# Kernel optimization log

Hardware: AMD Instinct MI355X
Metric: run time of the kernel (lower is better)

The kernel has to match this reference:

```python
import jax, jax.numpy as jnp
import numpy as np

_EPS = 1e-12  # torch F.normalize eps


def _normalize(x):
    # x: [B, N, 3]; matches torch.nn.functional.normalize(x, dim=2)
    norm = jnp.linalg.norm(x, axis=2, keepdims=True)
    return x / jnp.maximum(norm, _EPS)


def setup_inputs() -> dict:
    key = jax.random.key(0)
    k1, k2 = jax.random.split(key)
    xyz1 = jax.random.normal(k1, (8, 4096, 6), dtype=jnp.float32)
    xyz2 = jax.random.normal(k2, (8, 4096, 6), dtype=jnp.float32)
    return {"xyz1": xyz1, "xyz2": xyz2}


def reference(xyz1, xyz2):
    p1 = xyz1[:, :, :3]  # [B, N, 3]
    p2 = xyz2[:, :, :3]  # [B, M, 3]
    n1 = xyz1[:, :, 3:]  # [B, N, 3]
    n2 = xyz2[:, :, 3:]  # [B, M, 3]

    # Pairwise squared L2: |a|^2 + |b|^2 - 2 a.b  -> [B, N, M]
    sq1 = jnp.sum(p1 * p1, axis=2)  # [B, N]
    sq2 = jnp.sum(p2 * p2, axis=2)  # [B, M]
    cross = jnp.einsum('bnd,bmd->bnm', p1, p2)
    d = sq1[:, :, None] + sq2[:, None, :] - 2.0 * cross  # [B, N, M]

    dist1 = jnp.min(d, axis=2)      # [B, N] NN of each p1 in p2
    idx1 = jnp.argmin(d, axis=2)    # [B, N]
    dist2 = jnp.min(d, axis=1)      # [B, M] NN of each p2 in p1
    idx2 = jnp.argmin(d, axis=1)    # [B, M]

    # Gather matched normals
    t1 = jnp.take_along_axis(n2, idx1[:, :, None], axis=1)  # [B, N, 3]
    t2 = jnp.take_along_axis(n1, idx2[:, :, None], axis=1)  # [B, M, 3]

    nd1 = jnp.sum((_normalize(n1) - _normalize(t1)) ** 2, axis=2)  # [B, N]
    nd2 = jnp.sum((_normalize(n2) - _normalize(t2)) ** 2, axis=2)  # [B, M]

    return jnp.mean(dist1) + jnp.mean(dist2) + jnp.mean(nd1) + jnp.mean(nd2)
```

## Files before the change

kernel.cpp:

```cpp
#include <hip/hip_runtime.h>
#include <cstdint>

#define NB 8
#define NP 4096
#define THREADS 256
#define Q 4
#define CHUNK (THREADS * Q)
#define NCHUNK (NP / CHUNK)


template <int SEGV>
__global__ __launch_bounds__(THREADS) void chamfer_argmin(
    const float* __restrict__ xyz1, const float* __restrict__ xyz2,
    unsigned int* __restrict__ part)
{
    const int TSEG = NP / SEGV;
    __shared__ float4 tgt[NP / 16];

    unsigned int x = blockIdx.x;
    int seg   = x & (SEGV - 1);
    int chunk = (x / SEGV) & (NCHUNK - 1);
    int b     = (x / (SEGV * NCHUNK)) & 7;
    int dir   = x / (SEGV * NCHUNK * 8);

    const float* qset = dir ? xyz2 : xyz1;
    const float* tset = dir ? xyz1 : xyz2;

    int tbase = seg * TSEG;
    for (int t0 = threadIdx.x; t0 < TSEG; t0 += THREADS) {
        const float* src = tset + ((size_t)b * NP + tbase + t0) * 6;
        float tx = src[0], ty = src[1], tz = src[2];
        tgt[t0] = make_float4(tx, ty, tz, -0.5f * (tx * tx + ty * ty + tz * tz));
    }
    __syncthreads();

    float qx[Q], qy[Q], qz[Q], qq[Q], bs[Q];
    unsigned int bi[Q];
    int qbase = chunk * CHUNK + threadIdx.x;
    #pragma unroll
    for (int i = 0; i < Q; ++i) {
        const float* src = qset + ((size_t)b * NP + qbase + i * THREADS) * 6;
        qx[i] = src[0]; qy[i] = src[1]; qz[i] = src[2];
        qq[i] = qx[i] * qx[i] + qy[i] * qy[i] + qz[i] * qz[i];
        bs[i] = -3.4e38f;
        bi[i] = 0u;
    }

    #pragma unroll 4
    for (int k = 0; k < TSEG; ++k) {
        float4 t = tgt[k];
        unsigned int jb = (unsigned int)(tbase + k);
        #pragma unroll
        for (int i = 0; i < Q; ++i) {
            float s = fmaf(t.x, qx[i], fmaf(t.y, qy[i], fmaf(t.z, qz[i], t.w)));
            if (s > bs[i]) { bs[i] = s; bi[i] = jb; }
        }
    }

    unsigned int* slot =
        part + (((size_t)(dir * NB + b) * SEGV + seg) * NP) + qbase;
    #pragma unroll
    for (int i = 0; i < Q; ++i) {
        float d = fmaxf(fmaf(-2.0f, bs[i], qq[i]), 0.0f);
        slot[i * THREADS] = (__float_as_uint(d) & 0xFFFFF000u) | bi[i];
    }
}

template <int SEGV>
__global__ __launch_bounds__(256) void chamfer_finish(
    const float* __restrict__ xyz1, const float* __restrict__ xyz2,
    const unsigned int* __restrict__ part, float* __restrict__ out)
{
    int gid = blockIdx.x * 256 + threadIdx.x;
    int q   = gid & (NP - 1);
    int db  = gid >> 12;
    int b   = db & 7;
    int dir = db >> 3;

    const unsigned int* base = part + ((size_t)db * SEGV) * NP + q;
    unsigned int p = 0xFFFFFFFFu;
    #pragma unroll
    for (int s = 0; s < SEGV; ++s) p = min(p, base[(size_t)s * NP]);

    const float* qset = dir ? xyz2 : xyz1;
    const float* tset = dir ? xyz1 : xyz2;

    float dist = __uint_as_float(p & 0xFFFFF000u);
    int j = (int)(p & 0xFFFu);

    const float* nq = qset + ((size_t)b * NP + q) * 6 + 3;
    const float* nt = tset + ((size_t)b * NP + j) * 6 + 3;
    float ax = nq[0], ay = nq[1], az = nq[2];
    float bx = nt[0], by = nt[1], bz = nt[2];

    float na = fmaxf(sqrtf(ax * ax + ay * ay + az * az), 1e-12f);
    float nb = fmaxf(sqrtf(bx * bx + by * by + bz * bz), 1e-12f);
    float ra = 1.0f / na, rb = 1.0f / nb;
    float dx = ax * ra - bx * rb;
    float dy = ay * ra - by * rb;
    float dz = az * ra - bz * rb;
    float nd = dx * dx + dy * dy + dz * dz;

    float contrib = (dist + nd) * (1.0f / 32768.0f);

    for (int off = 32; off > 0; off >>= 1)
        contrib += __shfl_down(contrib, off, 64);
    __shared__ float wsum[4];
    if ((threadIdx.x & 63) == 0) wsum[threadIdx.x >> 6] = contrib;
    __syncthreads();
    if (threadIdx.x == 0)
        atomicAdd(out, wsum[0] + wsum[1] + wsum[2] + wsum[3]);
}

extern "C" void kernel_launch(void* const* d_in, const int* in_sizes, int n_in,
                              void* d_out, int out_size, void* d_ws, size_t ws_size,
                              hipStream_t stream) {
    const float* xyz1 = (const float*)d_in[0];
    const float* xyz2 = (const float*)d_in[1];
    float* out = (float*)d_out;
    unsigned int* part = (unsigned int*)d_ws;

    hipMemsetAsync(d_out, 0, sizeof(float), stream);

    size_t need32 = (size_t)2 * NB * 32 * NP * sizeof(unsigned int);
    if (ws_size >= need32) {
        chamfer_argmin<32><<<2 * NB * NCHUNK * 32, THREADS, 0, stream>>>(xyz1, xyz2, part);
        chamfer_finish<32><<<(2 * NB * NP) / 256, 256, 0, stream>>>(xyz1, xyz2, part, out);
    } else {
        chamfer_argmin<16><<<2 * NB * NCHUNK * 16, THREADS, 0, stream>>>(xyz1, xyz2, part);
        chamfer_finish<16><<<(2 * NB * NP) / 256, 256, 0, stream>>>(xyz1, xyz2, part, out);
    }
}
```

Measured before the change: 96.57 us.

## Group argmin over four targets with max-then-recover index; drop memset launch

The inner loop now takes the max over groups of four targets and stores only the group base index, then recomputes the four scores in the epilogue to find the exact winner. This cuts compare and select work per pair. Queries per thread go from four to eight, which halves the block count and raises register pressure. The output memset is replaced by a zero write inside the argmin kernel, removing one launch.

```diff
diff --git a/kernel.cpp b/kernel.cpp
--- a/kernel.cpp
+++ b/kernel.cpp
@@ -4,20 +4,22 @@
 #define NB 8
 #define NP 4096
 #define THREADS 256
-#define Q 4
+#define Q 8
 #define CHUNK (THREADS * Q)
 #define NCHUNK (NP / CHUNK)
+#define G 4
 
 
 template <int SEGV>
 __global__ __launch_bounds__(THREADS) void chamfer_argmin(
     const float* __restrict__ xyz1, const float* __restrict__ xyz2,
-    unsigned int* __restrict__ part)
+    unsigned int* __restrict__ part, float* __restrict__ out)
 {
     const int TSEG = NP / SEGV;
     __shared__ float4 tgt[NP / 16];
 
     unsigned int x = blockIdx.x;
+    if (x == 0 && threadIdx.x == 0) out[0] = 0.0f;
     int seg   = x & (SEGV - 1);
     int chunk = (x / SEGV) & (NCHUNK - 1);
     int b     = (x / (SEGV * NCHUNK)) & 7;
@@ -46,14 +48,20 @@
         bi[i] = 0u;
     }
 
-    #pragma unroll 4
-    for (int k = 0; k < TSEG; ++k) {
-        float4 t = tgt[k];
-        unsigned int jb = (unsigned int)(tbase + k);
+    #pragma unroll 2
+    for (int k = 0; k < TSEG; k += G) {
+        float4 t0 = tgt[k + 0];
+        float4 t1 = tgt[k + 1];
+        float4 t2 = tgt[k + 2];
+        float4 t3 = tgt[k + 3];
         #pragma unroll
         for (int i = 0; i < Q; ++i) {
-            float s = fmaf(t.x, qx[i], fmaf(t.y, qy[i], fmaf(t.z, qz[i], t.w)));
-            if (s > bs[i]) { bs[i] = s; bi[i] = jb; }
+            float s0 = fmaf(t0.x, qx[i], fmaf(t0.y, qy[i], fmaf(t0.z, qz[i], t0.w)));
+            float s1 = fmaf(t1.x, qx[i], fmaf(t1.y, qy[i], fmaf(t1.z, qz[i], t1.w)));
+            float s2 = fmaf(t2.x, qx[i], fmaf(t2.y, qy[i], fmaf(t2.z, qz[i], t2.w)));
+            float s3 = fmaf(t3.x, qx[i], fmaf(t3.y, qy[i], fmaf(t3.z, qz[i], t3.w)));
+            float m  = fmaxf(fmaxf(s0, s1), fmaxf(s2, s3));
+            if (m > bs[i]) { bs[i] = m; bi[i] = (unsigned int)k; }
         }
     }
 
@@ -61,8 +69,21 @@
         part + (((size_t)(dir * NB + b) * SEGV + seg) * NP) + qbase;
     #pragma unroll
     for (int i = 0; i < Q; ++i) {
+        int k = (int)bi[i];
+        float4 t0 = tgt[k + 0];
+        float4 t1 = tgt[k + 1];
+        float4 t2 = tgt[k + 2];
+        float4 t3 = tgt[k + 3];
+        float s0 = fmaf(t0.x, qx[i], fmaf(t0.y, qy[i], fmaf(t0.z, qz[i], t0.w)));
+        float s1 = fmaf(t1.x, qx[i], fmaf(t1.y, qy[i], fmaf(t1.z, qz[i], t1.w)));
+        float s2 = fmaf(t2.x, qx[i], fmaf(t2.y, qy[i], fmaf(t2.z, qz[i], t2.w)));
+        unsigned int j  = (unsigned int)(tbase + k);
+        unsigned int jj = j + 3;
+        jj = (s2 == bs[i]) ? j + 2 : jj;
+        jj = (s1 == bs[i]) ? j + 1 : jj;
+        jj = (s0 == bs[i]) ? j     : jj;
         float d = fmaxf(fmaf(-2.0f, bs[i], qq[i]), 0.0f);
-        slot[i * THREADS] = (__float_as_uint(d) & 0xFFFFF000u) | bi[i];
+        slot[i * THREADS] = (__float_as_uint(d) & 0xFFFFF000u) | jj;
     }
 }
 
@@ -120,14 +141,12 @@
     float* out = (float*)d_out;
     unsigned int* part = (unsigned int*)d_ws;
 
-    hipMemsetAsync(d_out, 0, sizeof(float), stream);
-
     size_t need32 = (size_t)2 * NB * 32 * NP * sizeof(unsigned int);
     if (ws_size >= need32) {
-        chamfer_argmin<32><<<2 * NB * NCHUNK * 32, THREADS, 0, stream>>>(xyz1, xyz2, part);
+        chamfer_argmin<32><<<2 * NB * NCHUNK * 32, THREADS, 0, stream>>>(xyz1, xyz2, part, out);
         chamfer_finish<32><<<(2 * NB * NP) / 256, 256, 0, stream>>>(xyz1, xyz2, part, out);
     } else {
-        chamfer_argmin<16><<<2 * NB * NCHUNK * 16, THREADS, 0, stream>>>(xyz1, xyz2, part);
+        chamfer_argmin<16><<<2 * NB * NCHUNK * 16, THREADS, 0, stream>>>(xyz1, xyz2, part, out);
         chamfer_finish<16><<<(2 * NB * NP) / 256, 256, 0, stream>>>(xyz1, xyz2, part, out);
     }
 }
```

After: 87.47 us. 9.4% less time.
